# Performance work log

Hardware: AMD Instinct MI355X
Metric: run time of the kernel (lower is better)

The kernel has to match this reference:

```python
import jax, jax.numpy as jnp
import numpy as np

B, C, H, W = 4, 96, 48, 48
N_STATE = 16
EXPAND = 2
D_INNER = EXPAND * C          # 192
DT_RANK = -(-C // 16)         # ceil(96/16) = 6
K = 4                         # 4 scan directions (VMamba cross-scan)
CA_R = 16                     # channel-attention reduction


def _ln(x, g, b, eps=1e-5):
    m = jnp.mean(x, -1, keepdims=True)
    v = jnp.mean((x - m) ** 2, -1, keepdims=True)
    return (x - m) * jax.lax.rsqrt(v + eps) * g + b


def setup_inputs() -> dict:
    key = jax.random.key(0)
    ks = jax.random.split(key, 12)
    f = lambda k, s, scale=0.02: jax.random.normal(k, s, dtype=jnp.float32) * scale
    # dt bias init per SS2D.dt_init: inv_dt = dt + log(-expm1(-dt))
    dt0 = jnp.exp(jax.random.uniform(ks[7], (K, D_INNER)) * (np.log(0.1) - np.log(1e-3)) + np.log(1e-3))
    dt_b = dt0 + jnp.log(-jnp.expm1(-dt0))
    A_logs = jnp.log(jnp.tile(jnp.arange(1, N_STATE + 1, dtype=jnp.float32)[None, :], (K * D_INNER, 1)))
    return {
        "x": jax.random.normal(ks[0], (B, C, H, W), dtype=jnp.float32),
        "ca_w1": f(ks[1], (C // CA_R, C), 0.1),
        "ca_w2": f(ks[2], (C, C // CA_R), 0.1),
        "ln_g": jnp.ones((C,), jnp.float32),
        "ln_b": jnp.zeros((C,), jnp.float32),
        "in_proj_w": f(ks[3], (2 * D_INNER, C)),
        "conv_w": f(ks[4], (D_INNER, 1, 3, 3), 0.1),
        "conv_b": jnp.zeros((D_INNER,), jnp.float32),
        "x_proj_w": f(ks[5], (K, DT_RANK + 2 * N_STATE, D_INNER)),
        "dt_w": f(ks[6], (K, D_INNER, DT_RANK), DT_RANK ** -0.5),
        "dt_b": dt_b,
        "A_logs": A_logs,
        "Ds": jnp.ones((K * D_INNER,), jnp.float32),
        "onorm_g": jnp.ones((D_INNER,), jnp.float32),
        "onorm_b": jnp.zeros((D_INNER,), jnp.float32),
        "out_proj_w": f(ks[8], (C, D_INNER)),
    }


def reference(x, ca_w1, ca_w2, ln_g, ln_b, in_proj_w, conv_w, conv_b,
              x_proj_w, dt_w, dt_b, A_logs, Ds, onorm_g, onorm_b, out_proj_w):
    # --- channel attention (SE-style) gating the encoder features ---
    s = x.mean((2, 3))                                    # [B,C]
    a = jax.nn.sigmoid(jax.nn.relu(s @ ca_w1.T) @ ca_w2.T)
    x_ca = x * a[:, :, None, None]

    # --- VSSBlock: LN -> SS2D -> residual ---
    xi = jnp.transpose(x_ca, (0, 2, 3, 1))               # [B,H,W,C]
    xn = _ln(xi, ln_g, ln_b)

    # SS2D in_proj, split x/z
    xz = xn @ in_proj_w.T                                 # [B,H,W,2*D]
    xc, z = jnp.split(xz, 2, axis=-1)

    # depthwise conv + SiLU
    xc = jnp.transpose(xc, (0, 3, 1, 2))                  # [B,D,H,W]
    xc = jax.lax.conv_general_dilated(
        xc, conv_w, (1, 1), 'SAME', feature_group_count=D_INNER,
        dimension_numbers=('NCHW', 'OIHW', 'NCHW')) + conv_b[None, :, None, None]
    xc = jax.nn.silu(xc)

    Bb, D, Hh, Ww = xc.shape
    L = Hh * Ww
    # cross-scan: hw, wh, and their reverses -> [B,4,D,L]
    x_hw = xc.reshape(Bb, D, L)
    x_wh = jnp.transpose(xc, (0, 1, 3, 2)).reshape(Bb, D, L)
    xs = jnp.stack([x_hw, x_wh], axis=1)
    xs = jnp.concatenate([xs, jnp.flip(xs, axis=-1)], axis=1)

    x_dbl = jnp.einsum('bkdl,kcd->bkcl', xs, x_proj_w)    # [B,4,R+2N,L]
    dts, Bs, Cs = jnp.split(x_dbl, [DT_RANK, DT_RANK + N_STATE], axis=2)
    dt = jnp.einsum('bkrl,kdr->bkdl', dts, dt_w)
    dt = jax.nn.softplus(dt + dt_b[None, :, :, None])     # [B,4,D,L]
    A = -jnp.exp(A_logs).reshape(K, D, N_STATE)           # [4,D,N]

    # selective scan over L (sequential recurrence, vectorized over B,K,D,N)
    dt_t = jnp.moveaxis(dt, -1, 0)                        # [L,B,4,D]
    B_t = jnp.moveaxis(Bs, -1, 0)                         # [L,B,4,N]
    C_t = jnp.moveaxis(Cs, -1, 0)
    u_t = jnp.moveaxis(xs, -1, 0)                         # [L,B,4,D]
    h0 = jnp.zeros((Bb, K, D, N_STATE), xc.dtype)

    def step(h, inp):
        dti, Bi, Ci, ui = inp
        h = h * jnp.exp(dti[..., None] * A) + (dti * ui)[..., None] * Bi[:, :, None, :]
        return h, jnp.einsum('bkdn,bkn->bkd', h, Ci)

    _, ys = jax.lax.scan(step, h0, (dt_t, B_t, C_t, u_t))
    ys = jnp.moveaxis(ys, 0, -1) + Ds.reshape(K, D)[None, :, :, None] * xs  # [B,4,D,L]

    # merge 4 directions back to hw order
    y_fwd, y_inv = ys[:, :2], jnp.flip(ys[:, 2:], axis=-1)

    def wh_to_hw(t):
        return jnp.transpose(t.reshape(Bb, D, Ww, Hh), (0, 1, 3, 2)).reshape(Bb, D, L)

    y = y_fwd[:, 0] + y_inv[:, 0] + wh_to_hw(y_fwd[:, 1]) + wh_to_hw(y_inv[:, 1])
    y = jnp.transpose(y.reshape(Bb, D, Hh, Ww), (0, 2, 3, 1))  # [B,H,W,D]
    y = _ln(y, onorm_g, onorm_b)
    y = y * jax.nn.silu(z)
    out = y @ out_proj_w.T                                # [B,H,W,C]
    out = xi + out                                        # VSSBlock residual
    return jnp.transpose(out, (0, 3, 1, 2))               # [B,C,H,W]
```

## Files before the change

### kernel.cpp

```cpp
#include <hip/hip_runtime.h>
#include <math.h>

#define Bn 4
#define Cc 96
#define Hh 48
#define Ww 48
#define HW 2304
#define Dd 192
#define NS 16
#define Kk 4
#define RK 6
#define CD 38
#define Ll 2304
#define NCH 32
#define CL 72
#define SU2S 72

typedef _Float16 half2v __attribute__((ext_vector_type(2)));
typedef _Float16 half4 __attribute__((ext_vector_type(4)));
typedef _Float16 half8 __attribute__((ext_vector_type(8)));
typedef float f4v __attribute__((ext_vector_type(4)));
typedef float f4raw __attribute__((ext_vector_type(4)));

#define FMA4(A,W,U) { A.x=fmaf(W,U.x,A.x); A.y=fmaf(W,U.y,A.y); A.z=fmaf(W,U.z,A.z); A.w=fmaf(W,U.w,A.w); }

__device__ __forceinline__ float sigmoidf_(float x){ return 1.0f/(1.0f+__expf(-x)); }
__device__ __forceinline__ float siluf_(float x){ return x*sigmoidf_(x); }
__device__ __forceinline__ float softplus_fast(float x){ return (x>15.0f)? x : __logf(1.0f+__expf(x)); }

__device__ __forceinline__ float dot2f(half2v a, half2v b, float c){
#if __has_builtin(__builtin_amdgcn_fdot2)
  return __builtin_amdgcn_fdot2(a, b, c, false);
#else
  return fmaf((float)a[1],(float)b[1], fmaf((float)a[0],(float)b[0], c));
#endif
}

__global__ __launch_bounds__(256) void k_mean(const float* __restrict__ x, float* __restrict__ s){
  int bc = blockIdx.x;
  const float* p = x + (size_t)bc*HW;
  float acc = 0.f;
  for(int i=threadIdx.x;i<HW;i+=256) acc += p[i];
  __shared__ float red[256];
  red[threadIdx.x]=acc; __syncthreads();
  for(int o=128;o>0;o>>=1){ if(threadIdx.x<o) red[threadIdx.x]+=red[threadIdx.x+o]; __syncthreads(); }
  if(threadIdx.x==0) s[bc]=red[0]*(1.0f/HW);
}

__global__ __launch_bounds__(384) void k_ca(const float* __restrict__ s, const float* __restrict__ w1,
                     const float* __restrict__ w2, float* __restrict__ a){
  __shared__ float hid[Bn*RK];
  int tid=threadIdx.x;
  if(tid<Bn*RK){
    int b=tid/RK, r=tid%RK;
    float acc=0.f;
    for(int c=0;c<Cc;c++) acc += s[b*Cc+c]*w1[r*Cc+c];
    hid[tid]=fmaxf(acc,0.f);
  }
  __syncthreads();
  int b=tid/Cc, c=tid%Cc;
  float acc=0.f;
  for(int r=0;r<RK;r++) acc += hid[b*RK+r]*w2[c*RK+r];
  a[tid]=sigmoidf_(acc);
}

__global__ __launch_bounds__(256) void k_xca(const float* __restrict__ x, const float* __restrict__ a,
                      float* __restrict__ xi){
  __shared__ float tile[32][65];
  int p0 = blockIdx.x*64, c0 = blockIdx.y*32, b = blockIdx.z;
  int pj = threadIdx.x%64, ci = threadIdx.x/64;
  for(int i=0;i<8;i++){
    int c = c0+ci+i*4;
    tile[ci+i*4][pj] = x[((size_t)(b*Cc+c))*HW + p0+pj]*a[b*Cc+c];
  }
  __syncthreads();
  int cl = threadIdx.x%32, pl = threadIdx.x/32;
  for(int i=0;i<8;i++){
    int p = pl + i*8;
    xi[((size_t)(b*HW + p0+p))*Cc + c0+cl] = tile[cl][p];
  }
}

__global__ __launch_bounds__(256) void k_lnproj(const float* __restrict__ xi,
    const float* __restrict__ g, const float* __restrict__ bta,
    const float* __restrict__ w, float* __restrict__ xc, float* __restrict__ z){
  __shared__ float su[Cc*36];
  __shared__ _Float16 wl16[128*104];
  int tid = threadIdx.x;
  int pix0 = blockIdx.x*32;
  int p = blockIdx.y;
  #pragma unroll
  for(int i=0;i<3;i++){
    int f4 = tid + 256*i;
    int px = f4/24, c4 = f4%24;
    float4 v = *(const float4*)(xi + (size_t)(pix0+px)*Cc + 4*c4);
    int sw = 4*(c4&7);
    su[(4*c4+0)*36 + (px^sw)] = v.x;
    su[(4*c4+1)*36 + (px^sw)] = v.y;
    su[(4*c4+2)*36 + (px^sw)] = v.z;
    su[(4*c4+3)*36 + (px^sw)] = v.w;
  }
  __syncthreads();
  {
    int px = tid>>3, gg = tid&7;
    float sm=0.f, sq=0.f;
    float vals[12];
    #pragma unroll
    for(int i=0;i<12;i++){
      int d = gg + 8*i;
      float v = su[d*36 + (px ^ (4*((d>>2)&7)))];
      vals[i]=v; sm+=v; sq+=v*v;
    }
    sm += __shfl_xor(sm,1); sq += __shfl_xor(sq,1);
    sm += __shfl_xor(sm,2); sq += __shfl_xor(sq,2);
    sm += __shfl_xor(sm,4); sq += __shfl_xor(sq,4);
    float mean = sm*(1.0f/Cc);
    float var  = sq*(1.0f/Cc) - mean*mean;
    float rs = rsqrtf(var + 1e-5f);
    #pragma unroll
    for(int i=0;i<12;i++){
      int d = gg + 8*i;
      su[d*36 + (px ^ (4*((d>>2)&7)))] = (vals[i]-mean)*rs*g[d] + bta[d];
    }
  }
  #pragma unroll
  for(int i=0;i<12;i++){
    int f4 = tid + 256*i;
    int r = f4/24, c4 = f4%24;
    float4 v = *(const float4*)(w + (size_t)(128*p + r)*Cc + 4*c4);
    half4 hv; hv[0]=(_Float16)v.x; hv[1]=(_Float16)v.y; hv[2]=(_Float16)v.z; hv[3]=(_Float16)v.w;
    *(half4*)(wl16 + r*104 + 4*c4) = hv;
  }
  __syncthreads();
  int t4 = tid&7, cg = tid>>3;
  float4 a0={0,0,0,0},a1={0,0,0,0},a2={0,0,0,0},a3={0,0,0,0};
  for(int d0=0; d0<Cc; d0+=8){
    half8 w0v = *(const half8*)(wl16 + (cg+  0)*104 + d0);
    half8 w1v = *(const half8*)(wl16 + (cg+ 32)*104 + d0);
    half8 w2v = *(const half8*)(wl16 + (cg+ 64)*104 + d0);
    half8 w3v = *(const half8*)(wl16 + (cg+ 96)*104 + d0);
    #pragma unroll
    for(int j=0;j<8;j++){
      int d = d0+j;
      float4 u4 = *(const float4*)(su + d*36 + 4*(t4 ^ ((d>>2)&7)));
      FMA4(a0,(float)w0v[j],u4);
      FMA4(a1,(float)w1v[j],u4);
      FMA4(a2,(float)w2v[j],u4);
      FMA4(a3,(float)w3v[j],u4);
    }
  }
  #pragma unroll
  for(int j=0;j<4;j++){
    int c = 128*p + cg + 32*j;
    float4 a = (j==0)?a0:(j==1)?a1:(j==2)?a2:a3;
    #pragma unroll
    for(int q=0;q<4;q++){
      int px = pix0 + 4*t4 + q;
      float vv = (q==0)?a.x:(q==1)?a.y:(q==2)?a.z:a.w;
      if(c < Dd) xc[(size_t)px*Dd + c] = vv;
      else       z [(size_t)px*Dd + (c-Dd)] = vv;
    }
  }
}

__global__ __launch_bounds__(256) void k_conv(const float* __restrict__ xc, const float* __restrict__ cw,
                       const float* __restrict__ cb, float* __restrict__ xo){
  int idx = blockIdx.x*256 + threadIdx.x;
  if(idx >= Bn*HW*(Dd/4)) return;
  int d4 = idx % (Dd/4); int pos = (idx/(Dd/4))%HW; int b = idx/((Dd/4)*HW);
  int h = pos/Ww, w = pos%Ww;
  int d0 = d4*4;
  float4 acc = {cb[d0],cb[d0+1],cb[d0+2],cb[d0+3]};
  #pragma unroll
  for(int kh=0;kh<3;kh++){
    int hh=h+kh-1; if(hh<0||hh>=Hh) continue;
    #pragma unroll
    for(int kw=0;kw<3;kw++){
      int ww2=w+kw-1; if(ww2<0||ww2>=Ww) continue;
      float4 v = *(const float4*)(xc + ((size_t)(b*HW + hh*Ww+ww2))*Dd + d0);
      int wi = kh*3+kw;
      acc.x += v.x*cw[(d0+0)*9+wi];
      acc.y += v.y*cw[(d0+1)*9+wi];
      acc.z += v.z*cw[(d0+2)*9+wi];
      acc.w += v.w*cw[(d0+3)*9+wi];
    }
  }
  float4 o; o.x=siluf_(acc.x); o.y=siluf_(acc.y); o.z=siluf_(acc.z); o.w=siluf_(acc.w);
  *(float4*)(xo + ((size_t)(b*HW+pos))*Dd + d0) = o;
}

__global__ __launch_bounds__(256) void k_xdbl(const float* __restrict__ xconv,
   const float* __restrict__ xpw, const float* __restrict__ dtw,
   const float* __restrict__ dtb, _Float16* __restrict__ dtT,
   _Float16* __restrict__ uT, float* __restrict__ BC){
  __shared__ _Float16 su2[96*SU2S];
  __shared__ _Float16 wl16[CD*200];
  __shared__ float dts[RK*36];
  int tid = threadIdx.x;
  int blk = blockIdx.x;
  int tile = blk % (Ll/32);
  int k    = (blk/(Ll/32))%Kk;
  int b    = blk/((Ll/32)*Kk);
  int ord  = k&1;
  bool rev = (k>=2);
  int t0 = tile*32;
  #pragma unroll
  for(int i=0;i<6;i++){
    int f4 = tid+256*i;
    int r = f4/48, c4 = f4%48;
    int t = t0+r;
    int pos = ord ? ((t%Ww)*Ww + t/Ww) : t;
    float4 v = *(const float4*)(xconv + (size_t)(b*HW+pos)*Dd + 4*c4);
    int dp0 = 2*c4;
    int off = ((r>>2) ^ (c4&7))*8 + (r&3)*2;
    half2v p0; p0[0]=(_Float16)v.x; p0[1]=(_Float16)v.y;
    half2v p1; p1[0]=(_Float16)v.z; p1[1]=(_Float16)v.w;
    *(half2v*)(su2 + dp0*SU2S + off) = p0;
    *(half2v*)(su2 + (dp0+1)*SU2S + off) = p1;
  }
  for(int i=tid;i<CD*48;i+=256){
    int c = i/48, c4 = i%48;
    float4 v = *(const float4*)(xpw + ((size_t)(k*CD+c))*Dd + 4*c4);
    half4 hv; hv[0]=(_Float16)v.x; hv[1]=(_Float16)v.y; hv[2]=(_Float16)v.z; hv[3]=(_Float16)v.w;
    *(half4*)(wl16 + c*200 + 4*c4) = hv;
  }
  __syncthreads();
  if(k<2 && tid < Dd){
    int d = tid;
    int dp = d>>1, par = d&1, swz = (dp>>1)&7;
    _Float16* up = uT + ((size_t)(b*2+ord)*Dd + d)*Ll + t0;
    #pragma unroll
    for(int r4=0;r4<8;r4++){
      half8 hv = *(const half8*)(su2 + dp*SU2S + (r4 ^ swz)*8);
      half4 o; o[0]=hv[0+par]; o[1]=hv[2+par]; o[2]=hv[4+par]; o[3]=hv[6+par];
      *(half4*)(up + 4*r4) = o;
    }
  }
  int t4 = tid&7, cg = tid>>3;
  bool has1 = (cg < CD-32);
  f4v a0={0,0,0,0}, a1={0,0,0,0};
  #pragma unroll 1
  for(int dpc=0; dpc<24; dpc++){
    f4raw w0r = *(const f4raw*)(wl16 + cg*200 + 8*dpc);
    f4raw w1r = {0.f,0.f,0.f,0.f};
    if(has1) w1r = *(const f4raw*)(wl16 + (cg+32)*200 + 8*dpc);
    #pragma unroll
    for(int j=0;j<4;j++){
      int dp = 4*dpc+j;
      f4raw ur = *(const f4raw*)(su2 + dp*SU2S + (t4 ^ ((dp>>1)&7))*8);
      half2v w0p = __builtin_bit_cast(half2v, w0r[j]);
      half2v w1p = __builtin_bit_cast(half2v, w1r[j]);
      #pragma unroll
      for(int q=0;q<4;q++){
        half2v up = __builtin_bit_cast(half2v, ur[q]);
        a0[q] = dot2f(up, w0p, a0[q]);
        if(has1) a1[q] = dot2f(up, w1p, a1[q]);
      }
    }
  }
  #pragma unroll
  for(int j=0;j<2;j++){
    if(j==1 && !has1) break;
    int c = cg + 32*j;
    f4v a = j? a1 : a0;
    if(c < RK){
      dts[c*36 + 4*t4+0]=a[0]; dts[c*36+4*t4+1]=a[1]; dts[c*36+4*t4+2]=a[2]; dts[c*36+4*t4+3]=a[3];
    } else {
      int nn = c - RK;
      float* dst = BC + ((size_t)(b*Kk+k)*Ll)*32 + nn;
      #pragma unroll
      for(int q=0;q<4;q++){
        int t = t0 + 4*t4 + q;
        int tq = rev ? (Ll-1-t) : t;
        dst[(size_t)tq*32] = a[q];
      }
    }
  }
  __syncthreads();
  int tl = tid&31, ds8 = tid>>5;
  #pragma unroll 4
  for(int i=0;i<24;i++){
    int d = ds8 + 8*i;
    float acc = dtb[k*Dd + d];
    #pragma unroll
    for(int r=0;r<RK;r++) acc = fmaf(dtw[((size_t)(k*Dd+d))*RK + r], dts[r*36 + tl], acc);
    acc = softplus_fast(acc);
    int tq = rev ? (Ll-1-t0-tl) : (t0+tl);
    dtT[((size_t)(b*Kk+k)*Dd + d)*Ll + tq] = (_Float16)acc;
  }
}

__global__ __launch_bounds__(256) void k_scan1(const _Float16* __restrict__ dtT,
  const _Float16* __restrict__ uT, const float* __restrict__ BC,
  const float* __restrict__ Alog, float* __restrict__ hloc, float* __restrict__ Pb){
  int blk=blockIdx.x;
  int dblk = blk % 3;
  int ch  = (blk/3)%NCH;
  int k   = (blk/(3*NCH))%Kk;
  int b   = blk/(3*NCH*Kk);
  int tid=threadIdx.x;
  int nq = tid&3, dl = tid>>2;
  int d = dblk*64 + dl;
  f4v An;
  #pragma unroll
  for(int i=0;i<4;i++) An[i] = -__expf(Alog[((size_t)(k*Dd+d))*NS + 4*nq + i]);
  const _Float16* dp = dtT + ((size_t)(b*Kk+k)*Dd + d)*Ll + ch*CL;
  const _Float16* ub = uT  + ((size_t)(b*2+(k&1))*Dd + d)*Ll;
  const float*    bc = BC  + ((size_t)(b*Kk+k)*Ll + ch*CL)*32 + 4*nq;
  bool rev = (k>=2);
  int s0 = ch*CL;
  f4v h = {0,0,0,0};
  float sdt = 0.f;
  for(int tl=0; tl<CL; tl+=4){
    half4 dt4 = *(const half4*)(dp+tl);
    float u[4];
    if(!rev){
      half4 u4 = *(const half4*)(ub + s0+tl);
      u[0]=(float)u4[0]; u[1]=(float)u4[1]; u[2]=(float)u4[2]; u[3]=(float)u4[3];
    } else {
      half4 u4 = *(const half4*)(ub + (Ll-4-s0-tl));
      u[0]=(float)u4[3]; u[1]=(float)u4[2]; u[2]=(float)u4[1]; u[3]=(float)u4[0];
    }
    #pragma unroll
    for(int j=0;j<4;j++){
      f4v Bv = *(const f4v*)(bc + (size_t)(tl+j)*32);
      float dtv = (float)dt4[j];
      sdt += dtv;
      float xB = dtv*u[j];
      #pragma unroll
      for(int i=0;i<4;i++){
        float ae = __expf(dtv*An[i]);
        h[i] = fmaf(h[i], ae, xB*Bv[i]);
      }
    }
  }
  size_t o = (((size_t)(b*Kk+k)*NCH + ch)*Dd + d)*NS + 4*nq;
  *(f4v*)(hloc + o) = h;
  f4v P;
  #pragma unroll
  for(int i=0;i<4;i++) P[i] = __expf(An[i]*sdt);
  *(f4v*)(Pb + o) = P;
}

__global__ __launch_bounds__(256) void k_comb(float* __restrict__ hloc,
  const float* __restrict__ Pb){
  int idx = blockIdx.x*256 + threadIdx.x;
  int inner = idx % (Dd*NS);
  int bk = idx / (Dd*NS);
  size_t base = (size_t)bk*NCH*Dd*NS + inner;
  float H = 0.f;
  for(int ch=0; ch<NCH; ch++){
    size_t o = base + (size_t)ch*Dd*NS;
    float hl = hloc[o];
    hloc[o] = H;
    H = Pb[o]*H + hl;
  }
}

__global__ __launch_bounds__(256) void k_scan2(const _Float16* __restrict__ dtT,
  const _Float16* __restrict__ uT, const float* __restrict__ BC,
  const float* __restrict__ Alog, const float* __restrict__ Ds,
  const float* __restrict__ Hin, float* __restrict__ yB){
  int blk=blockIdx.x;
  int dblk = blk % 3;
  int ch  = (blk/3)%NCH;
  int k   = (blk/(3*NCH))%Kk;
  int b   = blk/(3*NCH*Kk);
  int tid=threadIdx.x;
  int nq = tid&3, dl = tid>>2;
  int d = dblk*64 + dl;
  f4v An;
  #pragma unroll
  for(int i=0;i<4;i++) An[i] = -__expf(Alog[((size_t)(k*Dd+d))*NS + 4*nq + i]);
  float Dv = Ds[k*Dd+d];
  const _Float16* dp = dtT + ((size_t)(b*Kk+k)*Dd + d)*Ll + ch*CL;
  const _Float16* ub = uT  + ((size_t)(b*2+(k&1))*Dd + d)*Ll;
  const float*    bc = BC  + ((size_t)(b*Kk+k)*Ll + ch*CL)*32 + 4*nq;
  bool rev = (k>=2);
  int s0 = ch*CL;
  f4v h = *(const f4v*)(Hin + (((size_t)(b*Kk+k)*NCH + ch)*Dd + d)*NS + 4*nq);
  int lane = tid & 63;
  int wv = tid >> 6;
  int src = (lane&15)*4 + (lane>>4);
  float* ybase2 = yB + ((size_t)(b*Kk+k)*Ll + s0 + (lane>>4))*Dd + dblk*64 + wv*16 + (lane&15);
  for(int tl=0; tl<CL; tl+=4){
    half4 dt4 = *(const half4*)(dp+tl);
    float u[4];
    if(!rev){
      half4 u4 = *(const half4*)(ub + s0+tl);
      u[0]=(float)u4[0]; u[1]=(float)u4[1]; u[2]=(float)u4[2]; u[3]=(float)u4[3];
    } else {
      half4 u4 = *(const half4*)(ub + (Ll-4-s0-tl));
      u[0]=(float)u4[3]; u[1]=(float)u4[2]; u[2]=(float)u4[1]; u[3]=(float)u4[0];
    }
    float yreg = 0.f;
    #pragma unroll
    for(int j=0;j<4;j++){
      f4v Bv = *(const f4v*)(bc + (size_t)(tl+j)*32);
      f4v Cv = *(const f4v*)(bc + (size_t)(tl+j)*32 + 16);
      float dtv = (float)dt4[j];
      float xB = dtv*u[j];
      #pragma unroll
      for(int i=0;i<4;i++){
        float ae = __expf(dtv*An[i]);
        h[i] = fmaf(h[i], ae, xB*Bv[i]);
      }
      float p = h[0]*Cv[0];
      p = fmaf(h[1],Cv[1],p); p = fmaf(h[2],Cv[2],p); p = fmaf(h[3],Cv[3],p);
      p += __shfl_xor(p,1); p += __shfl_xor(p,2);
      if(nq==j) yreg = p + Dv*u[j];
    }
    float yout = __shfl(yreg, src);
    ybase2[(size_t)tl*Dd] = yout;
  }
}

__global__ __launch_bounds__(256) void k_merge(const float* __restrict__ yB,
  const float* __restrict__ og, const float* __restrict__ ob,
  const float* __restrict__ zB, const float* __restrict__ opw,
  const float* __restrict__ xi, float* __restrict__ ot){
  __shared__ float yv[Dd*36];
  __shared__ _Float16 wl16[48*200];
  int tid = threadIdx.x;
  int pix0 = blockIdx.x*32;
  int p = blockIdx.y;
  int b = pix0/HW;
  int pos0 = pix0%HW;
  size_t ybase = (size_t)b*Kk*Ll*Dd;
  #pragma unroll
  for(int i=0;i<6;i++){
    int f4 = tid+256*i;
    int r = f4/48, c4 = f4%48;
    int pos = pos0+r;
    int lwh = (pos%Ww)*Ww + pos/Ww;
    float4 v0 = *(const float4*)(yB + ybase + ((size_t)(0*Ll) + pos)*Dd + 4*c4);
    float4 v2 = *(const float4*)(yB + ybase + ((size_t)(2*Ll) + (Ll-1-pos))*Dd + 4*c4);
    float4 v1 = *(const float4*)(yB + ybase + ((size_t)(1*Ll) + lwh)*Dd + 4*c4);
    float4 v3 = *(const float4*)(yB + ybase + ((size_t)(3*Ll) + (Ll-1-lwh))*Dd + 4*c4);
    float4 v; v.x=v0.x+v1.x+v2.x+v3.x; v.y=v0.y+v1.y+v2.y+v3.y;
    v.z=v0.z+v1.z+v2.z+v3.z; v.w=v0.w+v1.w+v2.w+v3.w;
    int sw = 4*(c4&7);
    yv[(4*c4+0)*36 + (r^sw)] = v.x;
    yv[(4*c4+1)*36 + (r^sw)] = v.y;
    yv[(4*c4+2)*36 + (r^sw)] = v.z;
    yv[(4*c4+3)*36 + (r^sw)] = v.w;
  }
  for(int i=tid;i<48*48;i+=256){
    int c=i/48, c4=i%48;
    float4 v = *(const float4*)(opw + (size_t)(48*p+c)*Dd + 4*c4);
    half4 hv; hv[0]=(_Float16)v.x; hv[1]=(_Float16)v.y; hv[2]=(_Float16)v.z; hv[3]=(_Float16)v.w;
    *(half4*)(wl16 + c*200 + 4*c4) = hv;
  }
  __syncthreads();
  {
    int px = tid>>3, gg = tid&7;
    float sm=0.f, sq=0.f;
    float vals[24];
    #pragma unroll
    for(int i=0;i<24;i++){
      int d = gg + 8*i;
      float v = yv[d*36 + (px ^ (4*((d>>2)&7)))];
      vals[i]=v; sm+=v; sq+=v*v;
    }
    sm += __shfl_xor(sm,1); sq += __shfl_xor(sq,1);
    sm += __shfl_xor(sm,2); sq += __shfl_xor(sq,2);
    sm += __shfl_xor(sm,4); sq += __shfl_xor(sq,4);
    float mean = sm*(1.0f/Dd);
    float var  = sq*(1.0f/Dd) - mean*mean;
    float rs = rsqrtf(var + 1e-5f);
    #pragma unroll
    for(int i=0;i<24;i++){
      int d = gg + 8*i;
      float zv = zB[(size_t)(pix0+px)*Dd + d];
      yv[d*36 + (px ^ (4*((d>>2)&7)))] = ((vals[i]-mean)*rs*og[d] + ob[d]) * siluf_(zv);
    }
  }
  __syncthreads();
  int t4 = tid&7, cg = tid>>3;
  bool h1 = (cg < 16);
  float4 a0={0,0,0,0}, a1={0,0,0,0};
  for(int d0=0;d0<Dd;d0+=8){
    half8 w0v = *(const half8*)(wl16 + cg*200 + d0);
    half8 w1v;
    if(h1) w1v = *(const half8*)(wl16 + (cg+32)*200 + d0);
    #pragma unroll
    for(int j=0;j<8;j++){
      int d=d0+j;
      float4 u4 = *(const float4*)(yv + d*36 + 4*(t4 ^ ((d>>2)&7)));
      FMA4(a0,(float)w0v[j],u4);
      if(h1){ FMA4(a1,(float)w1v[j],u4); }
    }
  }
  #pragma unroll
  for(int j=0;j<2;j++){
    if(j==1 && !h1) break;
    int c = 48*p + cg + 32*j;
    float4 a = j?a1:a0;
    #pragma unroll
    for(int q=0;q<4;q++){
      int px = pix0 + 4*t4 + q;
      float vv = (q==0)?a.x:(q==1)?a.y:(q==2)?a.z:a.w;
      ot[(size_t)px*Cc + c] = vv + xi[(size_t)px*Cc + c];
    }
  }
}

__global__ __launch_bounds__(256) void k_outT(const float* __restrict__ ot, float* __restrict__ out){
  __shared__ float tile[64][33];
  int p0=blockIdx.x*64, c0=blockIdx.y*32, b=blockIdx.z;
  int cl=threadIdx.x%32, pl=threadIdx.x/32;
  for(int i=0;i<8;i++){
    int p = pl+i*8;
    tile[p][cl] = ot[((size_t)(b*HW+p0+p))*Cc + c0+cl];
  }
  __syncthreads();
  int pj=threadIdx.x%64, ci=threadIdx.x/64;
  for(int i=0;i<8;i++){
    int c=ci+i*4;
    out[((size_t)(b*Cc+c0+c))*HW + p0+pj] = tile[pj][c];
  }
}

extern "C" void kernel_launch(void* const* d_in, const int* in_sizes, int n_in,
                              void* d_out, int out_size, void* d_ws, size_t ws_size,
                              hipStream_t stream){
  const float* x   = (const float*)d_in[0];
  const float* cw1 = (const float*)d_in[1];
  const float* cw2 = (const float*)d_in[2];
  const float* lng = (const float*)d_in[3];
  const float* lnb = (const float*)d_in[4];
  const float* ipw = (const float*)d_in[5];
  const float* cvw = (const float*)d_in[6];
  const float* cvb = (const float*)d_in[7];
  const float* xpw = (const float*)d_in[8];
  const float* dtw = (const float*)d_in[9];
  const float* dtb = (const float*)d_in[10];
  const float* alg = (const float*)d_in[11];
  const float* ds  = (const float*)d_in[12];
  const float* ong = (const float*)d_in[13];
  const float* onb = (const float*)d_in[14];
  const float* opw = (const float*)d_in[15];
  float* out = (float*)d_out;
  float* ws = (float*)d_ws;

  float* s_   = ws;
  float* a_   = s_  + 384;
  float* xi_  = a_  + 384;
  float* xc_  = xi_ + 884736;
  float* z_   = xc_ + 1769472;
  float* xo_  = z_  + 1769472;
  _Float16* dtT_ = (_Float16*)(xo_ + 1769472);
  _Float16* uT_  = dtT_ + 7077888;
  float* BC_  = (float*)(uT_ + 3538944);
  float* yB_  = BC_ + 1179648;
  float* ot_  = yB_ + 7077888;

  float* hloc_ = xc_;
  float* Pb_   = xo_;

  k_mean  <<<Bn*Cc, 256, 0, stream>>>(x, s_);
  k_ca    <<<1, 384, 0, stream>>>(s_, cw1, cw2, a_);
  k_xca   <<<dim3(HW/64, Cc/32, Bn), 256, 0, stream>>>(x, a_, xi_);
  k_lnproj<<<dim3(Bn*HW/32, 3), 256, 0, stream>>>(xi_, lng, lnb, ipw, xc_, z_);
  k_conv  <<<(Bn*HW*(Dd/4))/256, 256, 0, stream>>>(xc_, cvw, cvb, xo_);
  k_xdbl  <<<Bn*Kk*(Ll/32), 256, 0, stream>>>(xo_, xpw, dtw, dtb, dtT_, uT_, BC_);
  k_scan1 <<<Bn*Kk*NCH*3, 256, 0, stream>>>(dtT_, uT_, BC_, alg, hloc_, Pb_);
  k_comb  <<<(Bn*Kk*Dd*NS)/256, 256, 0, stream>>>(hloc_, Pb_);
  k_scan2 <<<Bn*Kk*NCH*3, 256, 0, stream>>>(dtT_, uT_, BC_, alg, ds, hloc_, yB_);
  k_merge <<<dim3(Bn*HW/32, 2), 256, 0, stream>>>(yB_, ong, onb, z_, opw, xi_, ot_);
  k_outT  <<<dim3(HW/64, Cc/32, Bn), 256, 0, stream>>>(ot_, out);
}
```

Before: 189.4 us.

## Store B/C and scan outputs in fp16 and widen scan blocks to all channels

The B/C projection buffer and the per-direction scan output yB are now stored as fp16 instead of fp32. This halves the memory traffic in k_xdbl, both scan kernels and k_merge, and k_merge now reads them as half8. The scan kernels now use 768-thread blocks that cover all 192 channels of a chunk, so the B/C rows are shared across three times as many channels per block and there are fewer blocks. The trade-off is fp16 rounding of B, C and y, which adds some numerical error, plus fewer and larger blocks that change occupancy.

New measurement: 189.3 us. About the same (-0.0%).

```diff
diff --git a/kernel.cpp b/kernel.cpp
--- a/kernel.cpp
+++ b/kernel.cpp
@@ -192,7 +192,7 @@
 __global__ __launch_bounds__(256) void k_xdbl(const float* __restrict__ xconv,
    const float* __restrict__ xpw, const float* __restrict__ dtw,
    const float* __restrict__ dtb, _Float16* __restrict__ dtT,
-   _Float16* __restrict__ uT, float* __restrict__ BC){
+   _Float16* __restrict__ uT, _Float16* __restrict__ BC){
   __shared__ _Float16 su2[96*SU2S];
   __shared__ _Float16 wl16[CD*200];
   __shared__ float dts[RK*36];
@@ -267,12 +267,12 @@
       dts[c*36 + 4*t4+0]=a[0]; dts[c*36+4*t4+1]=a[1]; dts[c*36+4*t4+2]=a[2]; dts[c*36+4*t4+3]=a[3];
     } else {
       int nn = c - RK;
-      float* dst = BC + ((size_t)(b*Kk+k)*Ll)*32 + nn;
+      _Float16* dst = BC + ((size_t)(b*Kk+k)*Ll)*32 + nn;
       #pragma unroll
       for(int q=0;q<4;q++){
         int t = t0 + 4*t4 + q;
         int tq = rev ? (Ll-1-t) : t;
-        dst[(size_t)tq*32] = a[q];
+        dst[(size_t)tq*32] = (_Float16)a[q];
       }
     }
   }
@@ -290,23 +290,21 @@
   }
 }
 
-__global__ __launch_bounds__(256) void k_scan1(const _Float16* __restrict__ dtT,
-  const _Float16* __restrict__ uT, const float* __restrict__ BC,
+__global__ __launch_bounds__(768) void k_scan1(const _Float16* __restrict__ dtT,
+  const _Float16* __restrict__ uT, const _Float16* __restrict__ BC,
   const float* __restrict__ Alog, float* __restrict__ hloc, float* __restrict__ Pb){
   int blk=blockIdx.x;
-  int dblk = blk % 3;
-  int ch  = (blk/3)%NCH;
-  int k   = (blk/(3*NCH))%Kk;
-  int b   = blk/(3*NCH*Kk);
+  int ch  = blk%NCH;
+  int k   = (blk/NCH)%Kk;
+  int b   = blk/(NCH*Kk);
   int tid=threadIdx.x;
-  int nq = tid&3, dl = tid>>2;
-  int d = dblk*64 + dl;
+  int nq = tid&3, d = tid>>2;
   f4v An;
   #pragma unroll
   for(int i=0;i<4;i++) An[i] = -__expf(Alog[((size_t)(k*Dd+d))*NS + 4*nq + i]);
   const _Float16* dp = dtT + ((size_t)(b*Kk+k)*Dd + d)*Ll + ch*CL;
   const _Float16* ub = uT  + ((size_t)(b*2+(k&1))*Dd + d)*Ll;
-  const float*    bc = BC  + ((size_t)(b*Kk+k)*Ll + ch*CL)*32 + 4*nq;
+  const _Float16* bc = BC  + ((size_t)(b*Kk+k)*Ll + ch*CL)*32 + 4*nq;
   bool rev = (k>=2);
   int s0 = ch*CL;
   f4v h = {0,0,0,0};
@@ -323,14 +321,14 @@
     }
     #pragma unroll
     for(int j=0;j<4;j++){
-      f4v Bv = *(const f4v*)(bc + (size_t)(tl+j)*32);
+      half4 Bv = *(const half4*)(bc + (size_t)(tl+j)*32);
       float dtv = (float)dt4[j];
       sdt += dtv;
       float xB = dtv*u[j];
       #pragma unroll
       for(int i=0;i<4;i++){
         float ae = __expf(dtv*An[i]);
-        h[i] = fmaf(h[i], ae, xB*Bv[i]);
+        h[i] = fmaf(h[i], ae, xB*(float)Bv[i]);
       }
     }
   }
@@ -357,32 +355,30 @@
   }
 }
 
-__global__ __launch_bounds__(256) void k_scan2(const _Float16* __restrict__ dtT,
-  const _Float16* __restrict__ uT, const float* __restrict__ BC,
+__global__ __launch_bounds__(768) void k_scan2(const _Float16* __restrict__ dtT,
+  const _Float16* __restrict__ uT, const _Float16* __restrict__ BC,
   const float* __restrict__ Alog, const float* __restrict__ Ds,
-  const float* __restrict__ Hin, float* __restrict__ yB){
+  const float* __restrict__ Hin, _Float16* __restrict__ yB){
   int blk=blockIdx.x;
-  int dblk = blk % 3;
-  int ch  = (blk/3)%NCH;
-  int k   = (blk/(3*NCH))%Kk;
-  int b   = blk/(3*NCH*Kk);
+  int ch  = blk%NCH;
+  int k   = (blk/NCH)%Kk;
+  int b   = blk/(NCH*Kk);
   int tid=threadIdx.x;
-  int nq = tid&3, dl = tid>>2;
-  int d = dblk*64 + dl;
+  int nq = tid&3, d = tid>>2;
   f4v An;
   #pragma unroll
   for(int i=0;i<4;i++) An[i] = -__expf(Alog[((size_t)(k*Dd+d))*NS + 4*nq + i]);
   float Dv = Ds[k*Dd+d];
   const _Float16* dp = dtT + ((size_t)(b*Kk+k)*Dd + d)*Ll + ch*CL;
   const _Float16* ub = uT  + ((size_t)(b*2+(k&1))*Dd + d)*Ll;
-  const float*    bc = BC  + ((size_t)(b*Kk+k)*Ll + ch*CL)*32 + 4*nq;
+  const _Float16* bc = BC  + ((size_t)(b*Kk+k)*Ll + ch*CL)*32 + 4*nq;
   bool rev = (k>=2);
   int s0 = ch*CL;
   f4v h = *(const f4v*)(Hin + (((size_t)(b*Kk+k)*NCH + ch)*Dd + d)*NS + 4*nq);
   int lane = tid & 63;
   int wv = tid >> 6;
   int src = (lane&15)*4 + (lane>>4);
-  float* ybase2 = yB + ((size_t)(b*Kk+k)*Ll + s0 + (lane>>4))*Dd + dblk*64 + wv*16 + (lane&15);
+  _Float16* ybase2 = yB + ((size_t)(b*Kk+k)*Ll + s0 + (lane>>4))*Dd + wv*16 + (lane&15);
   for(int tl=0; tl<CL; tl+=4){
     half4 dt4 = *(const half4*)(dp+tl);
     float u[4];
@@ -396,26 +392,26 @@
     float yreg = 0.f;
     #pragma unroll
     for(int j=0;j<4;j++){
-      f4v Bv = *(const f4v*)(bc + (size_t)(tl+j)*32);
-      f4v Cv = *(const f4v*)(bc + (size_t)(tl+j)*32 + 16);
+      half4 Bv = *(const half4*)(bc + (size_t)(tl+j)*32);
+      half4 Cv = *(const half4*)(bc + (size_t)(tl+j)*32 + 16);
       float dtv = (float)dt4[j];
       float xB = dtv*u[j];
       #pragma unroll
       for(int i=0;i<4;i++){
         float ae = __expf(dtv*An[i]);
-        h[i] = fmaf(h[i], ae, xB*Bv[i]);
+        h[i] = fmaf(h[i], ae, xB*(float)Bv[i]);
       }
-      float p = h[0]*Cv[0];
-      p = fmaf(h[1],Cv[1],p); p = fmaf(h[2],Cv[2],p); p = fmaf(h[3],Cv[3],p);
+      float p = h[0]*(float)Cv[0];
+      p = fmaf(h[1],(float)Cv[1],p); p = fmaf(h[2],(float)Cv[2],p); p = fmaf(h[3],(float)Cv[3],p);
       p += __shfl_xor(p,1); p += __shfl_xor(p,2);
       if(nq==j) yreg = p + Dv*u[j];
     }
     float yout = __shfl(yreg, src);
-    ybase2[(size_t)tl*Dd] = yout;
-  }
-}
-
-__global__ __launch_bounds__(256) void k_merge(const float* __restrict__ yB,
+    ybase2[(size_t)tl*Dd] = (_Float16)yout;
+  }
+}
+
+__global__ __launch_bounds__(256) void k_merge(const _Float16* __restrict__ yB,
   const float* __restrict__ og, const float* __restrict__ ob,
   const float* __restrict__ zB, const float* __restrict__ opw,
   const float* __restrict__ xi, float* __restrict__ ot){
@@ -428,22 +424,21 @@
   int pos0 = pix0%HW;
   size_t ybase = (size_t)b*Kk*Ll*Dd;
   #pragma unroll
-  for(int i=0;i<6;i++){
-    int f4 = tid+256*i;
-    int r = f4/48, c4 = f4%48;
+  for(int i=0;i<3;i++){
+    int f8 = tid+256*i;
+    int r = f8/24, c8 = f8%24;
     int pos = pos0+r;
     int lwh = (pos%Ww)*Ww + pos/Ww;
-    float4 v0 = *(const float4*)(yB + ybase + ((size_t)(0*Ll) + pos)*Dd + 4*c4);
-    float4 v2 = *(const float4*)(yB + ybase + ((size_t)(2*Ll) + (Ll-1-pos))*Dd + 4*c4);
-    float4 v1 = *(const float4*)(yB + ybase + ((size_t)(1*Ll) + lwh)*Dd + 4*c4);
-    float4 v3 = *(const float4*)(yB + ybase + ((size_t)(3*Ll) + (Ll-1-lwh))*Dd + 4*c4);
-    float4 v; v.x=v0.x+v1.x+v2.x+v3.x; v.y=v0.y+v1.y+v2.y+v3.y;
-    v.z=v0.z+v1.z+v2.z+v3.z; v.w=v0.w+v1.w+v2.w+v3.w;
-    int sw = 4*(c4&7);
-    yv[(4*c4+0)*36 + (r^sw)] = v.x;
-    yv[(4*c4+1)*36 + (r^sw)] = v.y;
-    yv[(4*c4+2)*36 + (r^sw)] = v.z;
-    yv[(4*c4+3)*36 + (r^sw)] = v.w;
+    half8 v0 = *(const half8*)(yB + ybase + ((size_t)(0*Ll) + pos)*Dd + 8*c8);
+    half8 v2 = *(const half8*)(yB + ybase + ((size_t)(2*Ll) + (Ll-1-pos))*Dd + 8*c8);
+    half8 v1 = *(const half8*)(yB + ybase + ((size_t)(1*Ll) + lwh)*Dd + 8*c8);
+    half8 v3 = *(const half8*)(yB + ybase + ((size_t)(3*Ll) + (Ll-1-lwh))*Dd + 8*c8);
+    #pragma unroll
+    for(int j=0;j<8;j++){
+      int d = 8*c8+j;
+      float vs = (float)v0[j]+(float)v1[j]+(float)v2[j]+(float)v3[j];
+      yv[d*36 + (r ^ (4*((d>>2)&7)))] = vs;
+    }
   }
   for(int i=tid;i<48*48;i+=256){
     int c=i/48, c4=i%48;
@@ -551,9 +546,9 @@
   float* xo_  = z_  + 1769472;
   _Float16* dtT_ = (_Float16*)(xo_ + 1769472);
   _Float16* uT_  = dtT_ + 7077888;
-  float* BC_  = (float*)(uT_ + 3538944);
-  float* yB_  = BC_ + 1179648;
-  float* ot_  = yB_ + 7077888;
+  _Float16* BC_  = uT_ + 3538944;
+  _Float16* yB_  = BC_ + 1179648;
+  float* ot_  = (float*)(yB_ + 7077888);
 
   float* hloc_ = xc_;
   float* Pb_   = xo_;
@@ -564,9 +559,9 @@
   k_lnproj<<<dim3(Bn*HW/32, 3), 256, 0, stream>>>(xi_, lng, lnb, ipw, xc_, z_);
   k_conv  <<<(Bn*HW*(Dd/4))/256, 256, 0, stream>>>(xc_, cvw, cvb, xo_);
   k_xdbl  <<<Bn*Kk*(Ll/32), 256, 0, stream>>>(xo_, xpw, dtw, dtb, dtT_, uT_, BC_);
-  k_scan1 <<<Bn*Kk*NCH*3, 256, 0, stream>>>(dtT_, uT_, BC_, alg, hloc_, Pb_);
+  k_scan1 <<<Bn*Kk*NCH, 768, 0, stream>>>(dtT_, uT_, BC_, alg, hloc_, Pb_);
   k_comb  <<<(Bn*Kk*Dd*NS)/256, 256, 0, stream>>>(hloc_, Pb_);
-  k_scan2 <<<Bn*Kk*NCH*3, 256, 0, stream>>>(dtT_, uT_, BC_, alg, ds, hloc_, yB_);
+  k_scan2 <<<Bn*Kk*NCH, 768, 0, stream>>>(dtT_, uT_, BC_, alg, ds, hloc_, yB_);
   k_merge <<<dim3(Bn*HW/32, 2), 256, 0, stream>>>(yB_, ong, onb, z_, opw, xi_, ot_);
   k_outT  <<<dim3(HW/64, Cc/32, Bn), 256, 0, stream>>>(ot_, out);
 }
```
